# Performance work log

Hardware: AMD Instinct MI355X
Metric: run time of the kernel (lower is better)

Reference implementation:

```python
import jax, jax.numpy as jnp
import numpy as np

B, N, KD, VD, ID, H = 2, 2048, 1024, 1024, 1024, 16
HD = ID // H
SCALE = ID ** (-0.5)  # module quirk: scale uses inner_dim, not head_dim
EPS = 1e-5


def layernorm(x, g, b):
    mu = jnp.mean(x, axis=-1, keepdims=True)
    var = jnp.var(x, axis=-1, keepdims=True)
    return (x - mu) * jax.lax.rsqrt(var + EPS) * g + b


def setup_inputs() -> dict:
    key = jax.random.key(0)
    ks = jax.random.split(key, 12)
    d = {
        "keys": jax.random.normal(ks[0], (B, N, KD), jnp.float32),
        "values": jax.random.normal(ks[1], (B, N, VD), jnp.float32),
        "qk_norm_g": jnp.ones((KD,), jnp.float32),
        "qk_norm_b": jnp.zeros((KD,), jnp.float32),
        "value_norm_g": jnp.ones((VD,), jnp.float32),
        "value_norm_b": jnp.zeros((VD,), jnp.float32),
        "key_norm_g": jnp.ones((ID,), jnp.float32),
        "key_norm_b": jnp.zeros((ID,), jnp.float32),
        "query_norm_g": jnp.ones((ID,), jnp.float32),
        "query_norm_b": jnp.zeros((ID,), jnp.float32),
        "w_qk": jax.random.normal(ks[2], (KD, 2 * ID), jnp.float32) * (KD ** -0.5),
        "w_v": jax.random.normal(ks[3], (VD, ID), jnp.float32) * (VD ** -0.5),
        "w_out": jax.random.normal(ks[4], (ID, VD), jnp.float32) * (ID ** -0.5),
        "b_out": jnp.zeros((VD,), jnp.float32),
    }
    return d


def reference(keys, values, qk_norm_g, qk_norm_b, value_norm_g, value_norm_b,
              key_norm_g, key_norm_b, query_norm_g, query_norm_b,
              w_qk, w_v, w_out, b_out):
    keys = layernorm(keys, qk_norm_g, qk_norm_b)
    values = layernorm(values, value_norm_g, value_norm_b)
    qk = keys @ w_qk  # [B,N,2*ID]
    q, k = qk[..., :ID], qk[..., ID:]
    q = layernorm(q, query_norm_g, query_norm_b)
    k = layernorm(k, key_norm_g, key_norm_b)
    # b n (h d) -> b h n d
    q = q.reshape(B, N, H, HD).transpose(0, 2, 1, 3)
    k = k.reshape(B, N, H, HD).transpose(0, 2, 1, 3)
    v = (values @ w_v).reshape(B, N, H, HD).transpose(0, 2, 1, 3)
    dots = jnp.einsum('bhqd,bhkd->bhqk', q, k) * SCALE
    attn = jax.nn.softmax(dots, axis=-1)
    out = jnp.einsum('bhqk,bhkd->bhqd', attn, v)
    out = out.transpose(0, 2, 1, 3).reshape(B, N, ID)
    return out @ w_out + b_out
```

## Files before the change

kernel.cpp:

```cpp
#include <hip/hip_runtime.h>
#include <hip/hip_bf16.h>
#include <type_traits>


typedef __hip_bfloat16 bf16;
typedef __attribute__((ext_vector_type(8))) short bf16x8;
typedef __attribute__((ext_vector_type(4))) float f32x4;

#define MFMA_BF16(a, b, c) __builtin_amdgcn_mfma_f32_16x16x32_bf16((a), (b), (c), 0, 0, 0)

__device__ __forceinline__ float us2f(unsigned short u) {
  unsigned int v = ((unsigned int)u) << 16;
  return __builtin_bit_cast(float, v);
}

__device__ __forceinline__ unsigned pack_bf16x2(float a, float b) {
  union { __hip_bfloat162 h; unsigned u; } cv;
  cv.h = __float22bfloat162_rn(float2{a, b});
  return cv.u;
}

__device__ __forceinline__ unsigned pack_bf16x2_trunc(float a, float b) {
  return __builtin_amdgcn_perm(__builtin_bit_cast(unsigned, b),
                               __builtin_bit_cast(unsigned, a), 0x07060302u);
}

__device__ __forceinline__ void gl_lds16(const bf16* g, bf16* l) {
  __builtin_amdgcn_global_load_lds(
      (const __attribute__((address_space(1))) void*)g,
      (__attribute__((address_space(3))) void*)l, 16, 0, 0);
}

__device__ __forceinline__ void barrier_pinned() {
  __builtin_amdgcn_s_barrier();
  __builtin_amdgcn_sched_barrier(0);
}

__device__ __forceinline__ int xcd_swz(int orig, int nwg) {
  return (orig & 7) * (nwg >> 3) + (orig >> 3);
}

template <typename TIN>
__device__ __forceinline__ void ln_wave(
    const TIN* __restrict__ in, const float* __restrict__ gamma,
    const float* __restrict__ beta, bf16* __restrict__ out,
    int stride, float sc, int row)
{
  const int lane = threadIdx.x & 63;
  const TIN* rp = in + (size_t)row * stride;
  float x[16];
#pragma unroll
  for (int j = 0; j < 4; ++j) {
    if constexpr (std::is_same_v<TIN, float>) {
      float4 u = *(const float4*)(rp + j * 256 + lane * 4);
      x[j * 4 + 0] = u.x; x[j * 4 + 1] = u.y;
      x[j * 4 + 2] = u.z; x[j * 4 + 3] = u.w;
    } else {
      ushort4 u = *(const ushort4*)(rp + j * 256 + lane * 4);
      x[j * 4 + 0] = us2f(u.x); x[j * 4 + 1] = us2f(u.y);
      x[j * 4 + 2] = us2f(u.z); x[j * 4 + 3] = us2f(u.w);
    }
  }
  float s = 0.0f, s2 = 0.0f;
#pragma unroll
  for (int i = 0; i < 16; ++i) { s += x[i]; s2 += x[i] * x[i]; }
#pragma unroll
  for (int m = 1; m < 64; m <<= 1) {
    s += __shfl_xor(s, m);
    s2 += __shfl_xor(s2, m);
  }
  const float mu = s * (1.0f / 1024.0f);
  const float rs = rsqrtf(s2 * (1.0f / 1024.0f) - mu * mu + 1e-5f);
  bf16* op = out + (size_t)row * 1024;
#pragma unroll
  for (int j = 0; j < 4; ++j) {
    float4 g4 = *(const float4*)(gamma + j * 256 + lane * 4);
    float4 b4 = *(const float4*)(beta + j * 256 + lane * 4);
    uint2 o;
    o.x = pack_bf16x2(((x[j * 4 + 0] - mu) * rs * g4.x + b4.x) * sc,
                      ((x[j * 4 + 1] - mu) * rs * g4.y + b4.y) * sc);
    o.y = pack_bf16x2(((x[j * 4 + 2] - mu) * rs * g4.z + b4.z) * sc,
                      ((x[j * 4 + 3] - mu) * rs * g4.w + b4.w) * sc);
    *(uint2*)(op + j * 256 + lane * 4) = o;
  }
}

template <typename TIN>
__global__ __launch_bounds__(256) void ln2_kernel(
    const TIN* __restrict__ in0, const TIN* __restrict__ in1, int stride,
    const float* __restrict__ g0, const float* __restrict__ b0,
    const float* __restrict__ g1, const float* __restrict__ b1,
    bf16* __restrict__ out0, bf16* __restrict__ out1,
    float sc0, float sc1)
{
  const int w = threadIdx.x >> 6;
  const int lnid = blockIdx.x * 4 + w;
  const int row = lnid >> 1, which = lnid & 1;
  ln_wave<TIN>(which ? in1 : in0, which ? g1 : g0, which ? b1 : b0,
               which ? out1 : out0, stride, which ? sc1 : sc0, row);
}

__device__ __forceinline__ void transpose_core(
    const float* __restrict__ in, bf16* __restrict__ out, int C,
    int r0, int c0, float (*tile)[68])
{
  const int R = 1024;
  const int t = threadIdx.x;
  const int lr = t >> 2, lc = (t & 3) * 16;
  const float* src = in + (size_t)(r0 + lr) * C + (c0 + lc);
#pragma unroll
  for (int i = 0; i < 4; ++i) {
    float4 u = *(const float4*)(src + i * 4);
    tile[lr][lc + i * 4 + 0] = u.x;
    tile[lr][lc + i * 4 + 1] = u.y;
    tile[lr][lc + i * 4 + 2] = u.z;
    tile[lr][lc + i * 4 + 3] = u.w;
  }
  __syncthreads();
  __align__(16) bf16 tmp[16];
#pragma unroll
  for (int j = 0; j < 16; ++j) tmp[j] = __float2bfloat16(tile[lc + j][lr]);
  bf16* dst = out + (size_t)(c0 + lr) * R + (r0 + lc);
  *(bf16x8*)dst       = *(const bf16x8*)&tmp[0];
  *(bf16x8*)(dst + 8) = *(const bf16x8*)&tmp[8];
}

__global__ __launch_bounds__(256) void prep_kernel(
    const float* __restrict__ keys, const float* __restrict__ values,
    const float* __restrict__ qk_g, const float* __restrict__ qk_b,
    const float* __restrict__ val_g, const float* __restrict__ val_b,
    bf16* __restrict__ keys_ln, bf16* __restrict__ values_ln,
    const float* __restrict__ w_qk, bf16* __restrict__ wqkT,
    const float* __restrict__ w_v, bf16* __restrict__ wvT,
    const float* __restrict__ w_out, bf16* __restrict__ woutT)
{
  __shared__ float tile[64][68];
  const int bid = blockIdx.x;
  if (bid < 2048) {
    const int w = threadIdx.x >> 6;
    const int lnid = bid * 4 + w;
    const int row = lnid >> 1, which = lnid & 1;
    ln_wave<float>(which ? values : keys, which ? val_g : qk_g,
                   which ? val_b : qk_b, which ? values_ln : keys_ln,
                   1024, 1.0f, row);
  } else {
    const int tz = bid - 2048;
    if (tz < 512) {
      transpose_core(w_qk, wqkT, 2048, (tz >> 5) * 64, (tz & 31) * 64, tile);
    } else if (tz < 768) {
      const int s = tz - 512;
      transpose_core(w_v, wvT, 1024, (s >> 4) * 64, (s & 15) * 64, tile);
    } else {
      const int s = tz - 768;
      transpose_core(w_out, woutT, 1024, (s >> 4) * 64, (s & 15) * 64, tile);
    }
  }
}

template <int BM, int BN, int TMODE, typename TOUT>
__device__ __forceinline__ void gemm_core(
    const bf16* __restrict__ A, const bf16* __restrict__ Bt,
    const float* __restrict__ bias, TOUT* __restrict__ C,
    int N, int K, int has_bias, int bx, int by, bf16* smem)
{
  constexpr int MT = BM / 32, NT = BN / 32;
  constexpr int ASL = BM / 32, BSL = BN / 32;
  constexpr int BUFE = (BM + BN) * 64;
  const int t = threadIdx.x;
  const int w = t >> 6, lane = t & 63, l15 = lane & 15, quad = lane >> 4;
  const int wy = w >> 1, wx = w & 1;
  const bf16* Ab = A + (size_t)by * BM * K;
  const bf16* Bb = Bt + (size_t)bx * BN * K;
  f32x4 acc[MT][NT] = {};

  const bf16* aptr[ASL];
  const bf16* bptr[BSL];
#pragma unroll
  for (int i = 0; i < ASL; ++i) {
    int s = i * 256 + t, row = s >> 3, c = (s & 7) ^ (row & 7);
    aptr[i] = Ab + (size_t)row * K + (c << 3);
  }
#pragma unroll
  for (int i = 0; i < BSL; ++i) {
    int s = i * 256 + t, row = s >> 3, c = (s & 7) ^ (row & 7);
    bptr[i] = Bb + (size_t)row * K + (c << 3);
  }

  auto stage = [&](bf16* buf, int kc) {
#pragma unroll
    for (int i = 0; i < ASL; ++i)
      gl_lds16(aptr[i] + kc, buf + (i * 256 + t) * 8);
#pragma unroll
    for (int i = 0; i < BSL; ++i)
      gl_lds16(bptr[i] + kc, buf + BM * 64 + (i * 256 + t) * 8);
  };

  const int sw = (quad ^ (l15 & 7)) << 3;
  const int NK = K >> 6;

  stage(smem, 0);

  for (int kt = 0; kt < NK; ++kt) {
    const int cur = kt & 1;
    bf16* lA = smem + cur * BUFE;
    bf16* lB = lA + BM * 64;
    barrier_pinned();
    if (kt + 1 < NK) {
      stage(smem + (cur ^ 1) * BUFE, (kt + 1) << 6);
      if constexpr (ASL + BSL == 8)
        asm volatile("s_waitcnt vmcnt(8)" ::: "memory");
      else if constexpr (ASL + BSL == 6)
        asm volatile("s_waitcnt vmcnt(6)" ::: "memory");
      else
        asm volatile("s_waitcnt vmcnt(4)" ::: "memory");
    } else {
      asm volatile("s_waitcnt vmcnt(0)" ::: "memory");
    }
    barrier_pinned();

#pragma unroll
    for (int h = 0; h < 2; ++h) {
      const int so = sw ^ (h << 5);
      bf16x8 af[MT], bfr[NT];
#pragma unroll
      for (int mt = 0; mt < MT; ++mt)
        af[mt] = *(const bf16x8*)&lA[(wy * (BM / 2) + mt * 16 + l15) * 64 + so];
#pragma unroll
      for (int nt = 0; nt < NT; ++nt)
        bfr[nt] = *(const bf16x8*)&lB[(wx * (BN / 2) + nt * 16 + l15) * 64 + so];
#pragma unroll
      for (int mt = 0; mt < MT; ++mt)
#pragma unroll
        for (int nt = 0; nt < NT; ++nt)
          acc[mt][nt] = MFMA_BF16(af[mt], bfr[nt], acc[mt][nt]);
    }
  }

  if constexpr (TMODE == 1) {
    constexpr int STR = BM + 8;
    static_assert(BN * STR <= 2 * BUFE, "lOut must fit staging buffers");
    bf16* lOut = smem;
    __syncthreads();
#pragma unroll
    for (int mt = 0; mt < MT; ++mt)
#pragma unroll
      for (int nt = 0; nt < NT; ++nt) {
        const int d = wx * (BN / 2) + nt * 16 + l15;
        const int n = wy * (BM / 2) + mt * 16 + quad * 4;
        uint2 pk;
        pk.x = pack_bf16x2(acc[mt][nt][0], acc[mt][nt][1]);
        pk.y = pack_bf16x2(acc[mt][nt][2], acc[mt][nt][3]);
        *(uint2*)&lOut[d * STR + n] = pk;
      }
    __syncthreads();
    const int row0 = by * BM;
    const int bidx = row0 >> 11, n0 = row0 & 2047;
    const int col0 = bx * BN;
    constexpr int CPR = BM / 32;
    constexpr int NITER = (BN * CPR) / 256;
#pragma unroll
    for (int it = 0; it < NITER; ++it) {
      const int idx = it * 256 + t;
      const int d = idx / CPR, off = (idx % CPR) * 32;
      const bf16* srcp = &lOut[d * STR + off];
      bf16* g = (bf16*)C + ((size_t)(bidx << 10) + col0 + d) * 2048 + n0 + off;
#pragma unroll
      for (int j = 0; j < 4; ++j)
        *(bf16x8*)(g + j * 8) = *(const bf16x8*)(srcp + j * 8);
    }
  } else {
    const int row_base = by * BM + wy * (BM / 2);
    const int col_base = bx * BN + wx * (BN / 2);
#pragma unroll
    for (int mt = 0; mt < MT; ++mt)
#pragma unroll
      for (int nt = 0; nt < NT; ++nt) {
        const int col = col_base + nt * 16 + l15;
        const float bb = has_bias ? bias[col] : 0.0f;
#pragma unroll
        for (int r = 0; r < 4; ++r) {
          const int row = row_base + mt * 16 + quad * 4 + r;
          float v = acc[mt][nt][r] + bb;
          if constexpr (std::is_same_v<TOUT, bf16>)
            C[(size_t)row * N + col] = __float2bfloat16(v);
          else
            C[(size_t)row * N + col] = v;
        }
      }
  }
}

template <int BM, int BN, int TMODE, typename TOUT>
__global__ __launch_bounds__(256) void gemm_bt_kernel(
    const bf16* __restrict__ A, const bf16* __restrict__ Bt,
    const float* __restrict__ bias, TOUT* __restrict__ C,
    int N, int K, int has_bias)
{
  __shared__ __align__(16) bf16 smem[2 * (BM + BN) * 64];
  const int nwg = gridDim.x * gridDim.y;
  const int orig = blockIdx.y * gridDim.x + blockIdx.x;
  const int s = xcd_swz(orig, nwg);
  gemm_core<BM, BN, TMODE, TOUT>(A, Bt, bias, C, N, K, has_bias,
                                 s % gridDim.x, s / gridDim.x, smem);
}

__global__ __launch_bounds__(256) void gemm_dual_kernel(
    const bf16* __restrict__ A0, const bf16* __restrict__ B0, bf16* __restrict__ C0,
    const bf16* __restrict__ A1, const bf16* __restrict__ B1, bf16* __restrict__ C1)
{
  __shared__ __align__(16) bf16 smem[2 * 256 * 64];
  const int bid = blockIdx.x;
  if (bid < 512) {
    const int s = xcd_swz(bid, 512);
    gemm_core<128, 128, 0, bf16>(A0, B0, nullptr, C0, 2048, 1024, 0,
                                 s & 15, s >> 4, smem);
  } else {
    const int s = xcd_swz(bid - 512, 256);
    gemm_core<128, 128, 1, bf16>(A1, B1, nullptr, C1, 1024, 1024, 0,
                                 s & 7, s >> 3, smem);
  }
}

__global__ __launch_bounds__(256) void flash_kernel(
    const bf16* __restrict__ Q, const bf16* __restrict__ Km,
    const bf16* __restrict__ Vt, bf16* __restrict__ O)
{
  __shared__ __align__(16) bf16 smem[8192 + 16384 + 16384];
  bf16* lQ = smem;
  bf16* lKb = smem + 8192;
  bf16* lVb = smem + 8192 + 16384;
  const int t = threadIdx.x;
  const int w = t >> 6, lane = t & 63, l15 = lane & 15, quad = lane >> 4;
  const int bid = blockIdx.x;
  const int qt = (bid >> 3) & 15;
  const int bh = (bid & 7) + ((bid >> 7) << 3);
  const int b = bh >> 4, h = bh & 15;
  const int qrow0 = b * 2048 + qt * 128;
  const bf16* qbase = Q + (size_t)qrow0 * 1024 + h * 64;
  const bf16* kbase = Km + ((size_t)(b * 2048)) * 1024 + h * 64;
  const bf16* vbase = Vt + ((size_t)(b * 1024 + h * 64)) * 2048;

  const int sr0 = t >> 3, sc0 = ((t & 7) ^ (sr0 & 7)) << 3;
  const int sr1 = (256 + t) >> 3, sc1 = (((256 + t) & 7) ^ (sr1 & 7)) << 3;
  const int gr0 = (sr0 & 0x23) | ((sr0 & 0x0C) << 1) | ((sr0 & 0x10) >> 2);
  const int gr1 = (sr1 & 0x23) | ((sr1 & 0x0C) << 1) | ((sr1 & 0x10) >> 2);
  const bf16* kp0 = kbase + gr0 * 1024 + sc0;
  const bf16* kp1 = kbase + gr1 * 1024 + sc1;
  const bf16* vp0 = vbase + sr0 * 2048 + sc0;
  const bf16* vp1 = vbase + sr1 * 2048 + sc1;

  auto stage_kv = [&](bf16* kdst, bf16* vdst, int kro, int vco) {
    const int ko = kro << 10;
    gl_lds16(kp0 + ko, kdst + t * 8);
    gl_lds16(kp1 + ko, kdst + (256 + t) * 8);
    gl_lds16(vp0 + vco, vdst + t * 8);
    gl_lds16(vp1 + vco, vdst + (256 + t) * 8);
  };

#pragma unroll
  for (int i = 0; i < 4; ++i) {
    int s = i * 256 + t;
    int row = s >> 3, c = (s & 7) ^ (row & 7);
    gl_lds16(qbase + (size_t)row * 1024 + (c << 3), lQ + s * 8);
  }
  stage_kv(lKb, lVb, 0, 0);
  stage_kv(lKb + 4096, lVb + 4096, 64, 64);
  asm volatile("s_waitcnt vmcnt(8)" ::: "memory");
  barrier_pinned();

  const int sw = (quad ^ (l15 & 7)) << 3;
  bf16x8 qf[2][2];
#pragma unroll
  for (int mset = 0; mset < 2; ++mset) {
    const int row = w * 32 + mset * 16 + l15;
    qf[mset][0] = *(const bf16x8*)&lQ[row * 64 + sw];
    qf[mset][1] = *(const bf16x8*)&lQ[row * 64 + (sw ^ 32)];
  }

  f32x4 o_acc[4][2] = {};
  f32x4 s_acc[2] = {};
  const short ONEB = (short)0x3F80;
  const bf16x8 ones = {ONEB, ONEB, ONEB, ONEB, ONEB, ONEB, ONEB, ONEB};

  for (int kt = 0; kt < 16; ++kt) {
    const int cur = kt & 1;
    bf16* lK = lKb + cur * 8192;
    bf16* lV = lVb + cur * 8192;
    bf16* lKn = lKb + (cur ^ 1) * 8192;
    bf16* lVn = lVb + (cur ^ 1) * 8192;

    barrier_pinned();
    {
      const int ktn = (kt + 1) & 15;
      const int kro = ktn << 7;
      const int vco = ktn << 7;
      stage_kv(lKn, lVn, kro, vco);
      stage_kv(lKn + 4096, lVn + 4096, kro + 64, vco + 64);
    }
    asm volatile("s_waitcnt vmcnt(8)" ::: "memory");
    barrier_pinned();

#pragma unroll
    for (int sub = 0; sub < 2; ++sub) {
      bf16* lKs = lK + sub * 4096;
      bf16* lVs = lV + sub * 4096;

      bf16x8 kf[4][2];
#pragma unroll
      for (int nt = 0; nt < 4; ++nt) {
        kf[nt][0] = *(const bf16x8*)&lKs[(nt * 16 + l15) * 64 + sw];
        kf[nt][1] = *(const bf16x8*)&lKs[(nt * 16 + l15) * 64 + (sw ^ 32)];
      }

      bf16x8 pa[2][2];
#pragma unroll
      for (int mset = 0; mset < 2; ++mset) {
#pragma unroll
        for (int half = 0; half < 2; ++half) {
          f32x4 z0 = {}, z1 = {};
          z0 = MFMA_BF16(kf[2 * half + 0][0], qf[mset][0], z0);
          z0 = MFMA_BF16(kf[2 * half + 0][1], qf[mset][1], z0);
          z1 = MFMA_BF16(kf[2 * half + 1][0], qf[mset][0], z1);
          z1 = MFMA_BF16(kf[2 * half + 1][1], qf[mset][1], z1);
          f32x4 p0, p1;
#pragma unroll
          for (int r = 0; r < 4; ++r) {
            p0[r] = __builtin_amdgcn_exp2f(z0[r]);
            p1[r] = __builtin_amdgcn_exp2f(z1[r]);
          }
          union { unsigned u[4]; bf16x8 v; } cv;
          cv.u[0] = pack_bf16x2_trunc(p0[0], p0[1]);
          cv.u[1] = pack_bf16x2_trunc(p0[2], p0[3]);
          cv.u[2] = pack_bf16x2_trunc(p1[0], p1[1]);
          cv.u[3] = pack_bf16x2_trunc(p1[2], p1[3]);
          pa[mset][half] = cv.v;
        }
      }

      bf16x8 vf[4][2];
#pragma unroll
      for (int dt = 0; dt < 4; ++dt) {
        vf[dt][0] = *(const bf16x8*)&lVs[(dt * 16 + l15) * 64 + sw];
        vf[dt][1] = *(const bf16x8*)&lVs[(dt * 16 + l15) * 64 + (sw ^ 32)];
      }

      __builtin_amdgcn_s_setprio(1);
#pragma unroll
      for (int mset = 0; mset < 2; ++mset) {
        s_acc[mset] = MFMA_BF16(ones, pa[mset][0], s_acc[mset]);
        s_acc[mset] = MFMA_BF16(ones, pa[mset][1], s_acc[mset]);
#pragma unroll
        for (int dt = 0; dt < 4; ++dt) {
          o_acc[dt][mset] = MFMA_BF16(vf[dt][0], pa[mset][0], o_acc[dt][mset]);
          o_acc[dt][mset] = MFMA_BF16(vf[dt][1], pa[mset][1], o_acc[dt][mset]);
        }
      }
      __builtin_amdgcn_s_setprio(0);
    }
  }

#pragma unroll
  for (int mset = 0; mset < 2; ++mset) {
    const float inv = 1.0f / s_acc[mset][0];
    const int m = qrow0 + w * 32 + mset * 16 + l15;
#pragma unroll
    for (int dt = 0; dt < 4; ++dt) {
      uint2 ok;
      ok.x = pack_bf16x2(o_acc[dt][mset][0] * inv, o_acc[dt][mset][1] * inv);
      ok.y = pack_bf16x2(o_acc[dt][mset][2] * inv, o_acc[dt][mset][3] * inv);
      *(uint2*)&O[(size_t)m * 1024 + h * 64 + dt * 16 + quad * 4] = ok;
    }
  }
}

extern "C" void kernel_launch(void* const* d_in, const int* in_sizes, int n_in,
                              void* d_out, int out_size, void* d_ws, size_t ws_size,
                              hipStream_t stream)
{
  (void)in_sizes; (void)n_in; (void)out_size; (void)ws_size;
  const float* keys   = (const float*)d_in[0];
  const float* values = (const float*)d_in[1];
  const float* qk_g   = (const float*)d_in[2];
  const float* qk_b   = (const float*)d_in[3];
  const float* val_g  = (const float*)d_in[4];
  const float* val_b  = (const float*)d_in[5];
  const float* key_g  = (const float*)d_in[6];
  const float* key_b  = (const float*)d_in[7];
  const float* qry_g  = (const float*)d_in[8];
  const float* qry_b  = (const float*)d_in[9];
  const float* w_qk   = (const float*)d_in[10];
  const float* w_v    = (const float*)d_in[11];
  const float* w_out  = (const float*)d_in[12];
  const float* b_out  = (const float*)d_in[13];
  float* out = (float*)d_out;

  const float CEXP = 0.03125f * 1.44269504f;

  char* ws = (char*)d_ws;
  const size_t MB = 1024 * 1024;
  bf16* keys_ln   = (bf16*)(ws + 0);
  bf16* values_ln = (bf16*)(ws + 8 * MB);
  bf16* qk        = (bf16*)(ws + 16 * MB);
  bf16* vt        = (bf16*)(ws + 32 * MB);
  bf16* qln       = (bf16*)(ws + 0);
  bf16* kln       = (bf16*)(ws + 8 * MB);
  bf16* attn      = (bf16*)(ws + 16 * MB);
  bf16* wqkT      = (bf16*)(ws + 40 * MB);
  bf16* wvT       = (bf16*)(ws + 44 * MB);
  bf16* woutT     = (bf16*)(ws + 46 * MB);

  prep_kernel<<<dim3(3072), 256, 0, stream>>>(
      keys, values, qk_g, qk_b, val_g, val_b, keys_ln, values_ln,
      w_qk, wqkT, w_v, wvT, w_out, woutT);
  gemm_dual_kernel<<<dim3(768), 256, 0, stream>>>(
      keys_ln, wqkT, qk, values_ln, wvT, vt);
  ln2_kernel<bf16><<<dim3(2048), 256, 0, stream>>>(
      qk, qk + 1024, 2048, qry_g, qry_b, key_g, key_b, qln, kln, CEXP, 1.0f);
  flash_kernel<<<dim3(512), 256, 0, stream>>>(qln, kln, vt, attn);
  gemm_bt_kernel<128, 64, 0, float><<<dim3(16, 32), 256, 0, stream>>>(
      attn, woutT, b_out, out, 1024, 1024, 1);
}
```

Before: 208.9 us.

## Split flash attention KV range across waves with LDS reduction of partials

The flash kernel now assigns each block 64 query rows, up from 128, and launches twice as many blocks. Each wave processes a disjoint quarter of the key/value tiles for all 64 rows, staging its own K/V tile into a private LDS buffer with no block-wide barriers inside the loop. Partial outputs and row sums are combined through LDS at the end. The row sum moves from a ones-matrix MFMA to scalar adds. This is meant to raise parallelism and remove the per-iteration block synchronisation. The cost is losing double-buffered prefetch, because each wave waits on vmcnt(0) before computing, plus the extra reduction traffic.

```diff
diff --git a/kernel.cpp b/kernel.cpp
--- a/kernel.cpp
+++ b/kernel.cpp
@@ -325,150 +325,144 @@
     const bf16* __restrict__ Q, const bf16* __restrict__ Km,
     const bf16* __restrict__ Vt, bf16* __restrict__ O)
 {
-  __shared__ __align__(16) bf16 smem[8192 + 16384 + 16384];
+  __shared__ __align__(16) bf16 smem[4096 + 4 * 8192];
   bf16* lQ = smem;
-  bf16* lKb = smem + 8192;
-  bf16* lVb = smem + 8192 + 16384;
   const int t = threadIdx.x;
   const int w = t >> 6, lane = t & 63, l15 = lane & 15, quad = lane >> 4;
+  bf16* kbuf = smem + 4096 + w * 8192;
+  bf16* vbuf = kbuf + 4096;
   const int bid = blockIdx.x;
-  const int qt = (bid >> 3) & 15;
-  const int bh = (bid & 7) + ((bid >> 7) << 3);
+  const int qt = (bid >> 3) & 31;
+  const int bh = (bid & 7) + ((bid >> 8) << 3);
   const int b = bh >> 4, h = bh & 15;
-  const int qrow0 = b * 2048 + qt * 128;
+  const int qrow0 = b * 2048 + qt * 64;
   const bf16* qbase = Q + (size_t)qrow0 * 1024 + h * 64;
   const bf16* kbase = Km + ((size_t)(b * 2048)) * 1024 + h * 64;
   const bf16* vbase = Vt + ((size_t)(b * 1024 + h * 64)) * 2048;
 
-  const int sr0 = t >> 3, sc0 = ((t & 7) ^ (sr0 & 7)) << 3;
-  const int sr1 = (256 + t) >> 3, sc1 = (((256 + t) & 7) ^ (sr1 & 7)) << 3;
-  const int gr0 = (sr0 & 0x23) | ((sr0 & 0x0C) << 1) | ((sr0 & 0x10) >> 2);
-  const int gr1 = (sr1 & 0x23) | ((sr1 & 0x0C) << 1) | ((sr1 & 0x10) >> 2);
-  const bf16* kp0 = kbase + gr0 * 1024 + sc0;
-  const bf16* kp1 = kbase + gr1 * 1024 + sc1;
-  const bf16* vp0 = vbase + sr0 * 2048 + sc0;
-  const bf16* vp1 = vbase + sr1 * 2048 + sc1;
-
-  auto stage_kv = [&](bf16* kdst, bf16* vdst, int kro, int vco) {
-    const int ko = kro << 10;
-    gl_lds16(kp0 + ko, kdst + t * 8);
-    gl_lds16(kp1 + ko, kdst + (256 + t) * 8);
-    gl_lds16(vp0 + vco, vdst + t * 8);
-    gl_lds16(vp1 + vco, vdst + (256 + t) * 8);
-  };
-
-#pragma unroll
-  for (int i = 0; i < 4; ++i) {
+#pragma unroll
+  for (int i = 0; i < 2; ++i) {
     int s = i * 256 + t;
     int row = s >> 3, c = (s & 7) ^ (row & 7);
     gl_lds16(qbase + (size_t)row * 1024 + (c << 3), lQ + s * 8);
   }
-  stage_kv(lKb, lVb, 0, 0);
-  stage_kv(lKb + 4096, lVb + 4096, 64, 64);
-  asm volatile("s_waitcnt vmcnt(8)" ::: "memory");
+  asm volatile("s_waitcnt vmcnt(0)" ::: "memory");
   barrier_pinned();
 
   const int sw = (quad ^ (l15 & 7)) << 3;
-  bf16x8 qf[2][2];
-#pragma unroll
-  for (int mset = 0; mset < 2; ++mset) {
-    const int row = w * 32 + mset * 16 + l15;
-    qf[mset][0] = *(const bf16x8*)&lQ[row * 64 + sw];
-    qf[mset][1] = *(const bf16x8*)&lQ[row * 64 + (sw ^ 32)];
-  }
-
-  f32x4 o_acc[4][2] = {};
-  f32x4 s_acc[2] = {};
-  const short ONEB = (short)0x3F80;
-  const bf16x8 ones = {ONEB, ONEB, ONEB, ONEB, ONEB, ONEB, ONEB, ONEB};
-
-  for (int kt = 0; kt < 16; ++kt) {
-    const int cur = kt & 1;
-    bf16* lK = lKb + cur * 8192;
-    bf16* lV = lVb + cur * 8192;
-    bf16* lKn = lKb + (cur ^ 1) * 8192;
-    bf16* lVn = lVb + (cur ^ 1) * 8192;
-
-    barrier_pinned();
-    {
-      const int ktn = (kt + 1) & 15;
-      const int kro = ktn << 7;
-      const int vco = ktn << 7;
-      stage_kv(lKn, lVn, kro, vco);
-      stage_kv(lKn + 4096, lVn + 4096, kro + 64, vco + 64);
-    }
-    asm volatile("s_waitcnt vmcnt(8)" ::: "memory");
-    barrier_pinned();
-
-#pragma unroll
-    for (int sub = 0; sub < 2; ++sub) {
-      bf16* lKs = lK + sub * 4096;
-      bf16* lVs = lV + sub * 4096;
-
-      bf16x8 kf[4][2];
-#pragma unroll
-      for (int nt = 0; nt < 4; ++nt) {
-        kf[nt][0] = *(const bf16x8*)&lKs[(nt * 16 + l15) * 64 + sw];
-        kf[nt][1] = *(const bf16x8*)&lKs[(nt * 16 + l15) * 64 + (sw ^ 32)];
+  bf16x8 qf[4][2];
+#pragma unroll
+  for (int m = 0; m < 4; ++m) {
+    const int row = m * 16 + l15;
+    qf[m][0] = *(const bf16x8*)&lQ[row * 64 + sw];
+    qf[m][1] = *(const bf16x8*)&lQ[row * 64 + (sw ^ 32)];
+  }
+
+  const int hh = lane >> 3;
+  const int cK = ((lane & 7) ^ hh) << 3;
+  int gr[8];
+#pragma unroll
+  for (int i = 0; i < 8; ++i) {
+    int row = (i << 3) | hh;
+    gr[i] = (row & 0x23) | ((row & 0x0C) << 1) | ((row & 0x10) >> 2);
+  }
+
+  f32x4 o_acc[4][4] = {};
+  float l_sum[4] = {};
+
+  for (int j = 0; j < 8; ++j) {
+    const int kt = j * 4 + w;
+    const int kro = kt << 6;
+#pragma unroll
+    for (int i = 0; i < 8; ++i) {
+      gl_lds16(kbase + (size_t)(kro + gr[i]) * 1024 + cK, kbuf + i * 512 + lane * 8);
+      gl_lds16(vbase + (size_t)((i << 3) | hh) * 2048 + kro + cK, vbuf + i * 512 + lane * 8);
+    }
+    asm volatile("s_waitcnt vmcnt(0)" ::: "memory");
+    __builtin_amdgcn_sched_barrier(0);
+
+    bf16x8 kf[4][2];
+#pragma unroll
+    for (int nt = 0; nt < 4; ++nt) {
+      kf[nt][0] = *(const bf16x8*)&kbuf[(nt * 16 + l15) * 64 + sw];
+      kf[nt][1] = *(const bf16x8*)&kbuf[(nt * 16 + l15) * 64 + (sw ^ 32)];
+    }
+    bf16x8 vf[4][2];
+#pragma unroll
+    for (int dt = 0; dt < 4; ++dt) {
+      vf[dt][0] = *(const bf16x8*)&vbuf[(dt * 16 + l15) * 64 + sw];
+      vf[dt][1] = *(const bf16x8*)&vbuf[(dt * 16 + l15) * 64 + (sw ^ 32)];
+    }
+
+#pragma unroll
+    for (int m = 0; m < 4; ++m) {
+      bf16x8 pa[2];
+#pragma unroll
+      for (int half = 0; half < 2; ++half) {
+        f32x4 z0 = {}, z1 = {};
+        z0 = MFMA_BF16(kf[2 * half + 0][0], qf[m][0], z0);
+        z0 = MFMA_BF16(kf[2 * half + 0][1], qf[m][1], z0);
+        z1 = MFMA_BF16(kf[2 * half + 1][0], qf[m][0], z1);
+        z1 = MFMA_BF16(kf[2 * half + 1][1], qf[m][1], z1);
+        f32x4 p0, p1;
+#pragma unroll
+        for (int r = 0; r < 4; ++r) {
+          p0[r] = __builtin_amdgcn_exp2f(z0[r]);
+          p1[r] = __builtin_amdgcn_exp2f(z1[r]);
+        }
+        l_sum[m] += p0[0] + p0[1] + p0[2] + p0[3] + p1[0] + p1[1] + p1[2] + p1[3];
+        union { unsigned u[4]; bf16x8 v; } cv;
+        cv.u[0] = pack_bf16x2_trunc(p0[0], p0[1]);
+        cv.u[1] = pack_bf16x2_trunc(p0[2], p0[3]);
+        cv.u[2] = pack_bf16x2_trunc(p1[0], p1[1]);
+        cv.u[3] = pack_bf16x2_trunc(p1[2], p1[3]);
+        pa[half] = cv.v;
       }
-
-      bf16x8 pa[2][2];
-#pragma unroll
-      for (int mset = 0; mset < 2; ++mset) {
-#pragma unroll
-        for (int half = 0; half < 2; ++half) {
-          f32x4 z0 = {}, z1 = {};
-          z0 = MFMA_BF16(kf[2 * half + 0][0], qf[mset][0], z0);
-          z0 = MFMA_BF16(kf[2 * half + 0][1], qf[mset][1], z0);
-          z1 = MFMA_BF16(kf[2 * half + 1][0], qf[mset][0], z1);
-          z1 = MFMA_BF16(kf[2 * half + 1][1], qf[mset][1], z1);
-          f32x4 p0, p1;
-#pragma unroll
-          for (int r = 0; r < 4; ++r) {
-            p0[r] = __builtin_amdgcn_exp2f(z0[r]);
-            p1[r] = __builtin_amdgcn_exp2f(z1[r]);
-          }
-          union { unsigned u[4]; bf16x8 v; } cv;
-          cv.u[0] = pack_bf16x2_trunc(p0[0], p0[1]);
-          cv.u[1] = pack_bf16x2_trunc(p0[2], p0[3]);
-          cv.u[2] = pack_bf16x2_trunc(p1[0], p1[1]);
-          cv.u[3] = pack_bf16x2_trunc(p1[2], p1[3]);
-          pa[mset][half] = cv.v;
-        }
-      }
-
-      bf16x8 vf[4][2];
+      __builtin_amdgcn_s_setprio(1);
 #pragma unroll
       for (int dt = 0; dt < 4; ++dt) {
-        vf[dt][0] = *(const bf16x8*)&lVs[(dt * 16 + l15) * 64 + sw];
-        vf[dt][1] = *(const bf16x8*)&lVs[(dt * 16 + l15) * 64 + (sw ^ 32)];
-      }
-
-      __builtin_amdgcn_s_setprio(1);
-#pragma unroll
-      for (int mset = 0; mset < 2; ++mset) {
-        s_acc[mset] = MFMA_BF16(ones, pa[mset][0], s_acc[mset]);
-        s_acc[mset] = MFMA_BF16(ones, pa[mset][1], s_acc[mset]);
-#pragma unroll
-        for (int dt = 0; dt < 4; ++dt) {
-          o_acc[dt][mset] = MFMA_BF16(vf[dt][0], pa[mset][0], o_acc[dt][mset]);
-          o_acc[dt][mset] = MFMA_BF16(vf[dt][1], pa[mset][1], o_acc[dt][mset]);
-        }
+        o_acc[dt][m] = MFMA_BF16(vf[dt][0], pa[0], o_acc[dt][m]);
+        o_acc[dt][m] = MFMA_BF16(vf[dt][1], pa[1], o_acc[dt][m]);
       }
       __builtin_amdgcn_s_setprio(0);
     }
-  }
-
-#pragma unroll
-  for (int mset = 0; mset < 2; ++mset) {
-    const float inv = 1.0f / s_acc[mset][0];
-    const int m = qrow0 + w * 32 + mset * 16 + l15;
+
+    asm volatile("s_waitcnt lgkmcnt(0)" ::: "memory");
+    __builtin_amdgcn_sched_barrier(0);
+  }
+
+  __syncthreads();
+#pragma unroll
+  for (int m = 0; m < 4; ++m) {
+    float tm = l_sum[m];
+    tm += __shfl_xor(tm, 16);
+    tm += __shfl_xor(tm, 32);
+    if (quad == 0) ((float*)lQ)[(w * 4 + m) * 16 + l15] = tm;
+  }
+  float* part = (float*)(smem + 4096);
+#pragma unroll
+  for (int dt = 0; dt < 4; ++dt)
+#pragma unroll
+    for (int m = 0; m < 4; ++m)
+      *(f32x4*)&part[((w * 16 + dt * 4 + m) * 64 + lane) * 4] = o_acc[dt][m];
+  __syncthreads();
+  {
+    const int m = w;
+    const float* sums = (const float*)lQ;
+    const float tsum = sums[(0 * 4 + m) * 16 + l15] + sums[(1 * 4 + m) * 16 + l15] +
+                       sums[(2 * 4 + m) * 16 + l15] + sums[(3 * 4 + m) * 16 + l15];
+    const float inv = 1.0f / tsum;
+    const int mr = qrow0 + m * 16 + l15;
 #pragma unroll
     for (int dt = 0; dt < 4; ++dt) {
+      f32x4 o = *(const f32x4*)&part[((0 * 16 + dt * 4 + m) * 64 + lane) * 4];
+      o += *(const f32x4*)&part[((1 * 16 + dt * 4 + m) * 64 + lane) * 4];
+      o += *(const f32x4*)&part[((2 * 16 + dt * 4 + m) * 64 + lane) * 4];
+      o += *(const f32x4*)&part[((3 * 16 + dt * 4 + m) * 64 + lane) * 4];
       uint2 ok;
-      ok.x = pack_bf16x2(o_acc[dt][mset][0] * inv, o_acc[dt][mset][1] * inv);
-      ok.y = pack_bf16x2(o_acc[dt][mset][2] * inv, o_acc[dt][mset][3] * inv);
-      *(uint2*)&O[(size_t)m * 1024 + h * 64 + dt * 16 + quad * 4] = ok;
+      ok.x = pack_bf16x2(o[0] * inv, o[1] * inv);
+      ok.y = pack_bf16x2(o[2] * inv, o[3] * inv);
+      *(uint2*)&O[(size_t)mr * 1024 + h * 64 + dt * 16 + quad * 4] = ok;
     }
   }
 }
@@ -516,7 +510,7 @@
       keys_ln, wqkT, qk, values_ln, wvT, vt);
   ln2_kernel<bf16><<<dim3(2048), 256, 0, stream>>>(
       qk, qk + 1024, 2048, qry_g, qry_b, key_g, key_b, qln, kln, CEXP, 1.0f);
-  flash_kernel<<<dim3(512), 256, 0, stream>>>(qln, kln, vt, attn);
+  flash_kernel<<<dim3(1024), 256, 0, stream>>>(qln, kln, vt, attn);
   gemm_bt_kernel<128, 64, 0, float><<<dim3(16, 32), 256, 0, stream>>>(
       attn, woutT, b_out, out, 1024, 1024, 1);
 }
```

After: 237.6 us. 13.7% more time.
